# Kernel optimization log

Measured on AMD Instinct MI355X. Metric: run time of the kernel, lower is better.

The kernel has to match this reference:

```python
import jax, jax.numpy as jnp
import numpy as np

B, S, D, H = 2, 2048, 1024, 16
HD = D // H  # 64


def setup_inputs() -> dict:
    key = jax.random.key(0)
    ks = jax.random.split(key, 11)
    sc = 1.0 / np.sqrt(D)
    return {
        "query": jax.random.normal(ks[0], (B, S, D), jnp.float32),
        "key_in": jax.random.normal(ks[1], (B, S, D), jnp.float32),
        "value_in": jax.random.normal(ks[2], (B, S, D), jnp.float32),
        "mask": jnp.ones((1, 1, S, S), dtype=bool),
        "Wq": jax.random.normal(ks[3], (D, D), jnp.float32) * sc,
        "bq": jnp.zeros((D,), jnp.float32),
        "Wk": jax.random.normal(ks[4], (D, D), jnp.float32) * sc,
        "bk": jnp.zeros((D,), jnp.float32),
        "Wv": jax.random.normal(ks[5], (D, D), jnp.float32) * sc,
        "bv": jnp.zeros((D,), jnp.float32),
        "Wo": jax.random.normal(ks[6], (D, D), jnp.float32) * sc,
        "bo": jnp.zeros((D,), jnp.float32),
    }


def _split_heads(x):
    b, s, _ = x.shape
    return x.reshape(b, s, H, HD).transpose(0, 2, 1, 3)  # [B,H,S,HD]


def reference(query, key_in, value_in, mask, Wq, bq, Wk, bk, Wv, bv, Wo, bo):
    # linear projections (torch Linear: x @ W.T + b)
    q = _split_heads(query @ Wq.T + bq)
    k = _split_heads(key_in @ Wk.T + bk)
    v = _split_heads(value_in @ Wv.T + bv)
    scores = jnp.einsum("bhqd,bhkd->bhqk", q, k) / np.sqrt(HD).astype(np.float32)
    scores = jnp.where(mask == 0, jnp.float32(-1e20), scores)
    probs = jax.nn.softmax(scores, axis=-1)
    attn = jnp.einsum("bhqk,bhkd->bhqd", probs, v)  # [B,H,S,HD]
    combined = attn.transpose(0, 2, 1, 3).reshape(query.shape[0], query.shape[1], H * HD)
    return combined @ Wo.T + bo
```

## Files before the change

kernel.cpp:

```cpp
#include <hip/hip_runtime.h>

#define B_  2
#define S_  2048
#define D_  1024
#define H_  16
#define HD_ 64

typedef float          f32x4 __attribute__((ext_vector_type(4)));
typedef short          s16x8 __attribute__((ext_vector_type(8)));
typedef unsigned short u16x4 __attribute__((ext_vector_type(4)));

static __device__ __forceinline__ unsigned short f2bf(float f) {
  unsigned int u = __builtin_bit_cast(unsigned int, f);
  u += 0x7FFFu + ((u >> 16) & 1u);
  return (unsigned short)(u >> 16);
}

#define GLDS16(g, l)                                                        \
  __builtin_amdgcn_global_load_lds(                                         \
      (const __attribute__((address_space(1))) void*)(g),                   \
      (__attribute__((address_space(3))) void*)(l), 16, 0, 0)

#define XF(r) (((((r) >> 4) & 3) * 16) ^ ((((r) & 7)) * 8))
#define XP(r) ((((r) >> 2) & 3) * 16)

struct ConvSet {
  const float* s[7];
  unsigned short* d[7];
  int n[7];
};

__global__ __launch_bounds__(256) void conv_kernel(ConvSet cs) {
  const int idx = blockIdx.y;
  const int i = (blockIdx.x * 256 + threadIdx.x) * 8;
  if (i >= cs.n[idx]) return;
  const float* s = cs.s[idx];
  unsigned short* d = cs.d[idx];
  f32x4 a = *(const f32x4*)(s + i);
  f32x4 b = *(const f32x4*)(s + i + 4);
  u16x4 pa, pb;
#pragma unroll
  for (int j = 0; j < 4; ++j) { pa[j] = f2bf(a[j]); pb[j] = f2bf(b[j]); }
  *(u16x4*)(d + i) = pa;
  *(u16x4*)(d + i + 4) = pb;
}

template <bool PERM>
__global__ __launch_bounds__(256) void gemm_bf16(
    const unsigned short* __restrict__ X0, const unsigned short* __restrict__ X1,
    const unsigned short* __restrict__ X2,
    const unsigned short* __restrict__ W0, const unsigned short* __restrict__ W1,
    const unsigned short* __restrict__ W2,
    const float* __restrict__ b0, const float* __restrict__ b1, const float* __restrict__ b2,
    void* __restrict__ o0, void* __restrict__ o1, void* __restrict__ o2)
{
  constexpr int K = D_, N = D_;
  const int z = blockIdx.z;
  const unsigned short* X = z == 0 ? X0 : (z == 1 ? X1 : X2);
  const unsigned short* W = z == 0 ? W0 : (z == 1 ? W1 : W2);
  const float* bias       = z == 0 ? b0 : (z == 1 ? b1 : b2);
  void* outp              = z == 0 ? o0 : (z == 1 ? o1 : o2);

  __shared__ unsigned short As[128][32];
  __shared__ unsigned short Bs[128][32];

  const int t = threadIdx.x, lane = t & 63, w = t >> 6;
  const int wr = w >> 1, wc = w & 1;
  const int m0 = blockIdx.y * 128, n0 = blockIdx.x * 128;
  const int lg = lane >> 4, lr = lane & 15;

  const int srow = w * 32 + (lane >> 2);
  const int scol = (lane & 3) * 8;
  const unsigned short* Asrc = X + (size_t)(m0 + srow) * K + scol;
  const unsigned short* Bsrc = W + (size_t)(n0 + srow) * K + scol;

  f32x4 acc[4][4];
#pragma unroll
  for (int i = 0; i < 4; ++i)
#pragma unroll
    for (int j = 0; j < 4; ++j) acc[i][j] = f32x4{0.f, 0.f, 0.f, 0.f};

  for (int k0 = 0; k0 < K; k0 += 32) {
    __syncthreads();
#pragma unroll
    for (int i = 0; i < 2; ++i) {
      GLDS16(Asrc + k0 + (size_t)i * 16 * K, &As[w * 32 + i * 16][0]);
      GLDS16(Bsrc + k0 + (size_t)i * 16 * K, &Bs[w * 32 + i * 16][0]);
    }
    __syncthreads();

    s16x8 af[4], bfr[4];
#pragma unroll
    for (int i = 0; i < 4; ++i) af[i]  = *(const s16x8*)&As[wr * 64 + i * 16 + lr][lg * 8];
#pragma unroll
    for (int j = 0; j < 4; ++j) bfr[j] = *(const s16x8*)&Bs[wc * 64 + j * 16 + lr][lg * 8];
#pragma unroll
    for (int i = 0; i < 4; ++i)
#pragma unroll
      for (int j = 0; j < 4; ++j)
        acc[i][j] = __builtin_amdgcn_mfma_f32_16x16x32_bf16(af[i], bfr[j], acc[i][j], 0, 0, 0);
  }

#pragma unroll
  for (int i = 0; i < 4; ++i) {
    int rowb = m0 + wr * 64 + i * 16 + lg * 4;
#pragma unroll
    for (int j = 0; j < 4; ++j) {
      int col = n0 + wc * 64 + j * 16 + lr;
      float bv = bias[col];
#pragma unroll
      for (int r = 0; r < 4; ++r) {
        float v = acc[i][j][r] + bv;
        int rr = rowb + r;
        if (PERM) {
          int b = rr >> 11, s = rr & (S_ - 1);
          int h = col >> 6, hd = col & (HD_ - 1);
          ((unsigned short*)outp)[(((size_t)(b * H_ + h)) * S_ + s) * HD_ + hd] = f2bf(v);
        } else {
          ((float*)outp)[(size_t)rr * N + col] = v;
        }
      }
    }
  }
}

template <bool XF32, bool PERM>
__global__ __launch_bounds__(256) void gemm_kernel(
    const void* __restrict__ X0, const void* __restrict__ X1, const void* __restrict__ X2,
    const float* __restrict__ W0, const float* __restrict__ W1, const float* __restrict__ W2,
    const float* __restrict__ b0, const float* __restrict__ b1, const float* __restrict__ b2,
    void* __restrict__ o0, void* __restrict__ o1, void* __restrict__ o2)
{
  constexpr int K = D_, N = D_;
  const int z = blockIdx.z;
  const void*  Xv   = z == 0 ? X0 : (z == 1 ? X1 : X2);
  const float* W    = z == 0 ? W0 : (z == 1 ? W1 : W2);
  const float* bias = z == 0 ? b0 : (z == 1 ? b1 : b2);
  void*        outp = z == 0 ? o0 : (z == 1 ? o1 : o2);

  __shared__ unsigned short As[128][32];
  __shared__ unsigned short Bs[128][32];

  const int t = threadIdx.x, lane = t & 63, w = t >> 6;
  const int wr = w >> 1, wc = w & 1;
  const int m0 = blockIdx.y * 128, n0 = blockIdx.x * 128;
  const int lg = lane >> 4, lr = lane & 15;

  f32x4 acc[4][4];
#pragma unroll
  for (int i = 0; i < 4; ++i)
#pragma unroll
    for (int j = 0; j < 4; ++j) acc[i][j] = f32x4{0.f, 0.f, 0.f, 0.f};

  for (int k0 = 0; k0 < K; k0 += 32) {
    __syncthreads();
#pragma unroll
    for (int i = 0; i < 4; ++i) {
      int c = t + 256 * i;
      int row = c >> 3, ko = (c & 7) * 4;
      if (XF32) {
        const float* Xf = (const float*)Xv;
        f32x4 v = *(const f32x4*)(Xf + (size_t)(m0 + row) * K + k0 + ko);
        u16x4 p;
#pragma unroll
        for (int j = 0; j < 4; ++j) p[j] = f2bf(v[j]);
        *(u16x4*)&As[row][ko] = p;
      } else {
        const unsigned short* Xu = (const unsigned short*)Xv;
        *(u16x4*)&As[row][ko] = *(const u16x4*)(Xu + (size_t)(m0 + row) * K + k0 + ko);
      }
    }
#pragma unroll
    for (int i = 0; i < 4; ++i) {
      int c = t + 256 * i;
      int row = c >> 3, ko = (c & 7) * 4;
      f32x4 v = *(const f32x4*)(W + (size_t)(n0 + row) * K + k0 + ko);
      u16x4 p;
#pragma unroll
      for (int j = 0; j < 4; ++j) p[j] = f2bf(v[j]);
      *(u16x4*)&Bs[row][ko] = p;
    }
    __syncthreads();

    s16x8 af[4], bfr[4];
#pragma unroll
    for (int i = 0; i < 4; ++i) af[i]  = *(const s16x8*)&As[wr * 64 + i * 16 + lr][lg * 8];
#pragma unroll
    for (int j = 0; j < 4; ++j) bfr[j] = *(const s16x8*)&Bs[wc * 64 + j * 16 + lr][lg * 8];
#pragma unroll
    for (int i = 0; i < 4; ++i)
#pragma unroll
      for (int j = 0; j < 4; ++j)
        acc[i][j] = __builtin_amdgcn_mfma_f32_16x16x32_bf16(af[i], bfr[j], acc[i][j], 0, 0, 0);
  }

#pragma unroll
  for (int i = 0; i < 4; ++i) {
    int rowb = m0 + wr * 64 + i * 16 + lg * 4;
#pragma unroll
    for (int j = 0; j < 4; ++j) {
      int col = n0 + wc * 64 + j * 16 + lr;
      float bv = bias[col];
#pragma unroll
      for (int r = 0; r < 4; ++r) {
        float v = acc[i][j][r] + bv;
        int rr = rowb + r;
        if (PERM) {
          int b = rr >> 11, s = rr & (S_ - 1);
          int h = col >> 6, hd = col & (HD_ - 1);
          ((unsigned short*)outp)[(((size_t)(b * H_ + h)) * S_ + s) * HD_ + hd] = f2bf(v);
        } else {
          ((float*)outp)[(size_t)rr * N + col] = v;
        }
      }
    }
  }
}

__global__ __launch_bounds__(256) void attn_kernel(
    const unsigned short* __restrict__ Q,
    const unsigned short* __restrict__ Kg,
    const unsigned short* __restrict__ V,
    unsigned short* __restrict__ O)
{
  __shared__ unsigned short Ks[64][64];
  __shared__ unsigned short Vt[64][64];
  __shared__ unsigned short Pw[4][16][64];

  const int t = threadIdx.x, lane = t & 63, w = t >> 6;
  const int lg = lane >> 4, lr = lane & 15;
  const int bh = blockIdx.y;
  const int q0 = blockIdx.x * 64 + w * 16;
  const size_t base = (size_t)bh * S_ * HD_;

  s16x8 qa[2];
#pragma unroll
  for (int kc = 0; kc < 2; ++kc)
    qa[kc] = *(const s16x8*)(Q + base + (size_t)(q0 + lr) * HD_ + kc * 32 + lg * 8);

  const int cg = (lane & 7) ^ ((w & 3) * 2) ^ ((lane >> 3) & 7);
  const unsigned short* Ksrc0 =
      Kg + base + (size_t)(w * 16 + (lane >> 3)) * HD_ + cg * 8;

  const int sr = t >> 2;
  const int sc = (t & 3) * 16;
  const unsigned short* Vsrc0 = V + base + (size_t)sr * HD_ + sc;
  int vcol0[8], vcol1[8];
#pragma unroll
  for (int j = 0; j < 8; ++j) {
    vcol0[j] = sr ^ XF(sc + j);
    vcol1[j] = sr ^ XF(sc + 8 + j);
  }

  f32x4 po[4];
#pragma unroll
  for (int nb = 0; nb < 4; ++nb) po[nb] = f32x4{0.f, 0.f, 0.f, 0.f};
  float m_r[4], l_r[4];
#pragma unroll
  for (int r = 0; r < 4; ++r) { m_r[r] = -1e30f; l_r[r] = 0.f; }

  const float C2 = 0.18033688f;

  for (int kt = 0; kt < S_ / 64; ++kt) {
    __syncthreads();
    {
      const size_t toff = (size_t)kt * 64 * HD_;
      GLDS16(Ksrc0 + toff, &Ks[w * 16][0]);
      GLDS16(Ksrc0 + toff + 8 * HD_, &Ks[w * 16 + 8][0]);
      s16x8 v0 = *(const s16x8*)(Vsrc0 + toff);
      s16x8 v1 = *(const s16x8*)(Vsrc0 + toff + 8);
#pragma unroll
      for (int j = 0; j < 8; ++j) {
        Vt[sc + j][vcol0[j]]     = (unsigned short)v0[j];
        Vt[sc + 8 + j][vcol1[j]] = (unsigned short)v1[j];
      }
    }
    __syncthreads();

    f32x4 sf[4];
#pragma unroll
    for (int nb = 0; nb < 4; ++nb) {
      f32x4 a = f32x4{0.f, 0.f, 0.f, 0.f};
      int row = nb * 16 + lr;
      int xr = XF(row);
#pragma unroll
      for (int kc = 0; kc < 2; ++kc) {
        s16x8 kb = *(const s16x8*)&Ks[row][(kc * 32 + lg * 8) ^ xr];
        a = __builtin_amdgcn_mfma_f32_16x16x32_bf16(qa[kc], kb, a, 0, 0, 0);
      }
      sf[nb] = a;
    }

    float pr[4][4], mx[4];
#pragma unroll
    for (int r = 0; r < 4; ++r) {
      float s0 = sf[0][r] * C2, s1 = sf[1][r] * C2;
      float s2 = sf[2][r] * C2, s3 = sf[3][r] * C2;
      pr[0][r] = s0; pr[1][r] = s1; pr[2][r] = s2; pr[3][r] = s3;
      mx[r] = fmaxf(fmaxf(s0, s1), fmaxf(s2, s3));
    }
#pragma unroll
    for (int off = 8; off >= 1; off >>= 1)
#pragma unroll
      for (int r = 0; r < 4; ++r) mx[r] = fmaxf(mx[r], __shfl_xor(mx[r], off));

    bool grow = false;
#pragma unroll
    for (int r = 0; r < 4; ++r) grow = grow || (mx[r] > m_r[r] + 8.f);
    if (__any(grow)) {
#pragma unroll
      for (int r = 0; r < 4; ++r) {
        float mn = fmaxf(m_r[r], mx[r]);
        float alpha = __builtin_amdgcn_exp2f(m_r[r] - mn);
        m_r[r] = mn;
        l_r[r] *= alpha;
#pragma unroll
        for (int nb = 0; nb < 4; ++nb) po[nb][r] *= alpha;
      }
    }

    float rs[4];
#pragma unroll
    for (int r = 0; r < 4; ++r) {
      float a0 = __builtin_amdgcn_exp2f(pr[0][r] - m_r[r]);
      float a1 = __builtin_amdgcn_exp2f(pr[1][r] - m_r[r]);
      float a2 = __builtin_amdgcn_exp2f(pr[2][r] - m_r[r]);
      float a3 = __builtin_amdgcn_exp2f(pr[3][r] - m_r[r]);
      pr[0][r] = a0; pr[1][r] = a1; pr[2][r] = a2; pr[3][r] = a3;
      rs[r] = (a0 + a1) + (a2 + a3);
    }
#pragma unroll
    for (int off = 8; off >= 1; off >>= 1)
#pragma unroll
      for (int r = 0; r < 4; ++r) rs[r] += __shfl_xor(rs[r], off);
#pragma unroll
    for (int r = 0; r < 4; ++r) l_r[r] += rs[r];

#pragma unroll
    for (int nb = 0; nb < 4; ++nb)
#pragma unroll
      for (int r = 0; r < 4; ++r) {
        int row = lg * 4 + r;
        Pw[w][row][(nb * 16 + lr) ^ XP(row)] = f2bf(pr[nb][r]);
      }
    asm volatile("s_waitcnt lgkmcnt(0)" ::: "memory");
    __builtin_amdgcn_sched_barrier(0);
    s16x8 pa[2];
#pragma unroll
    for (int kc = 0; kc < 2; ++kc)
      pa[kc] = *(const s16x8*)&Pw[w][lr][(kc * 32 + lg * 8) ^ XP(lr)];

#pragma unroll
    for (int nb = 0; nb < 4; ++nb) {
      int d = nb * 16 + lr;
      int xd = XF(d);
#pragma unroll
      for (int kc = 0; kc < 2; ++kc) {
        s16x8 vb = *(const s16x8*)&Vt[d][(kc * 32 + lg * 8) ^ xd];
        po[nb] = __builtin_amdgcn_mfma_f32_16x16x32_bf16(pa[kc], vb, po[nb], 0, 0, 0);
      }
    }
  }

  const int b = bh >> 4, h = bh & (H_ - 1);
  float inv[4];
#pragma unroll
  for (int r = 0; r < 4; ++r) inv[r] = __builtin_amdgcn_rcpf(l_r[r]);
#pragma unroll
  for (int nb = 0; nb < 4; ++nb)
#pragma unroll
    for (int r = 0; r < 4; ++r) {
      int q = q0 + lg * 4 + r;
      int d = nb * 16 + lr;
      O[((size_t)(b * S_ + q)) * D_ + h * HD_ + d] = f2bf(po[nb][r] * inv[r]);
    }
}

extern "C" void kernel_launch(void* const* d_in, const int* in_sizes, int n_in,
                              void* d_out, int out_size, void* d_ws, size_t ws_size,
                              hipStream_t stream) {
  const float* query    = (const float*)d_in[0];
  const float* key_in   = (const float*)d_in[1];
  const float* value_in = (const float*)d_in[2];
  const float* Wq = (const float*)d_in[4];
  const float* bq = (const float*)d_in[5];
  const float* Wk = (const float*)d_in[6];
  const float* bk = (const float*)d_in[7];
  const float* Wv = (const float*)d_in[8];
  const float* bv = (const float*)d_in[9];
  const float* Wo = (const float*)d_in[10];
  const float* bo = (const float*)d_in[11];

  const size_t NA = (size_t)B_ * S_ * D_;
  const size_t NW = (size_t)D_ * D_;
  dim3 blk(256);

  if (ws_size >= (7 * NA + 4 * NW) * sizeof(unsigned short)) {
    unsigned short* Xb[3];
    Xb[0] = (unsigned short*)d_ws;
    Xb[1] = Xb[0] + NA;
    Xb[2] = Xb[1] + NA;
    unsigned short* Wb[4];
    Wb[0] = Xb[2] + NA;
    Wb[1] = Wb[0] + NW;
    Wb[2] = Wb[1] + NW;
    Wb[3] = Wb[2] + NW;
    unsigned short* Qp = Wb[3] + NW;
    unsigned short* Kp = Qp + NA;
    unsigned short* Vp = Kp + NA;
    unsigned short* Ao = Vp + NA;

    ConvSet cs;
    cs.s[0] = query;    cs.d[0] = Xb[0]; cs.n[0] = (int)NA;
    cs.s[1] = key_in;   cs.d[1] = Xb[1]; cs.n[1] = (int)NA;
    cs.s[2] = value_in; cs.d[2] = Xb[2]; cs.n[2] = (int)NA;
    cs.s[3] = Wq; cs.d[3] = Wb[0]; cs.n[3] = (int)NW;
    cs.s[4] = Wk; cs.d[4] = Wb[1]; cs.n[4] = (int)NW;
    cs.s[5] = Wv; cs.d[5] = Wb[2]; cs.n[5] = (int)NW;
    cs.s[6] = Wo; cs.d[6] = Wb[3]; cs.n[6] = (int)NW;
    conv_kernel<<<dim3((unsigned)(NA / (256 * 8)), 7), blk, 0, stream>>>(cs);

    gemm_bf16<true><<<dim3(8, 32, 3), blk, 0, stream>>>(
        Xb[0], Xb[1], Xb[2], Wb[0], Wb[1], Wb[2], bq, bk, bv, Qp, Kp, Vp);
    attn_kernel<<<dim3(S_ / 64, B_ * H_), blk, 0, stream>>>(Qp, Kp, Vp, Ao);
    gemm_bf16<false><<<dim3(8, 32, 1), blk, 0, stream>>>(
        Ao, nullptr, nullptr, Wb[3], nullptr, nullptr, bo, nullptr, nullptr,
        (float*)d_out, nullptr, nullptr);
  } else {
    unsigned short* Qp = (unsigned short*)d_ws;
    unsigned short* Kp = Qp + NA;
    unsigned short* Vp = Kp + NA;
    unsigned short* Ao = Vp + NA;
    gemm_kernel<true, true><<<dim3(8, 32, 3), blk, 0, stream>>>(
        query, key_in, value_in, Wq, Wk, Wv, bq, bk, bv, Qp, Kp, Vp);
    attn_kernel<<<dim3(S_ / 64, B_ * H_), blk, 0, stream>>>(Qp, Kp, Vp, Ao);
    gemm_kernel<false, false><<<dim3(8, 32, 1), blk, 0, stream>>>(
        Ao, nullptr, nullptr, Wo, nullptr, nullptr, bo, nullptr, nullptr,
        (float*)d_out, nullptr, nullptr);
  }
}
```

Before: 305.8 us.

## Fuse activation bf16 conversion into QKV GEMM, pre-transpose V, double-buffer attention

The QKV projection GEMM now reads fp32 activations directly and converts them to bf16 while staging into shared memory. This removes the separate conversion pass over the three activation tensors and its workspace traffic. The V projection is written transposed ([d][s]), so the attention kernel can load V tiles asynchronously with global_load_lds instead of scattering a transpose through LDS. Attention now double-buffers its K/V tiles, swaps MFMA operand order so each lane owns one query row (simplifying max/sum reductions), and packs P stores and the output write through LDS for coalesced 16-byte global stores. The fallback gemm_kernel's epilogue was also changed so its V output is transposed, which the fallback attention path now expects. The trade-offs are uncoalesced fp32 activation loads in the GEMM main loop and more LDS use in attention.

```diff
diff --git a/kernel.cpp b/kernel.cpp
--- a/kernel.cpp
+++ b/kernel.cpp
@@ -9,6 +9,7 @@
 typedef float          f32x4 __attribute__((ext_vector_type(4)));
 typedef short          s16x8 __attribute__((ext_vector_type(8)));
 typedef unsigned short u16x4 __attribute__((ext_vector_type(4)));
+typedef unsigned int   u32x4 __attribute__((ext_vector_type(4)));
 
 static __device__ __forceinline__ unsigned short f2bf(float f) {
   unsigned int u = __builtin_bit_cast(unsigned int, f);
@@ -21,13 +22,10 @@
       (const __attribute__((address_space(1))) void*)(g),                   \
       (__attribute__((address_space(3))) void*)(l), 16, 0, 0)
 
-#define XF(r) (((((r) >> 4) & 3) * 16) ^ ((((r) & 7)) * 8))
-#define XP(r) ((((r) >> 2) & 3) * 16)
-
 struct ConvSet {
-  const float* s[7];
-  unsigned short* d[7];
-  int n[7];
+  const float* s[4];
+  unsigned short* d[4];
+  int n[4];
 };
 
 __global__ __launch_bounds__(256) void conv_kernel(ConvSet cs) {
@@ -45,10 +43,10 @@
   *(u16x4*)(d + i + 4) = pb;
 }
 
-template <bool PERM>
+template <int XM, bool PERM>
 __global__ __launch_bounds__(256) void gemm_bf16(
-    const unsigned short* __restrict__ X0, const unsigned short* __restrict__ X1,
-    const unsigned short* __restrict__ X2,
+    const void* __restrict__ X0, const void* __restrict__ X1,
+    const void* __restrict__ X2,
     const unsigned short* __restrict__ W0, const unsigned short* __restrict__ W1,
     const unsigned short* __restrict__ W2,
     const float* __restrict__ b0, const float* __restrict__ b1, const float* __restrict__ b2,
@@ -56,7 +54,7 @@
 {
   constexpr int K = D_, N = D_;
   const int z = blockIdx.z;
-  const unsigned short* X = z == 0 ? X0 : (z == 1 ? X1 : X2);
+  const void* X           = z == 0 ? X0 : (z == 1 ? X1 : X2);
   const unsigned short* W = z == 0 ? W0 : (z == 1 ? W1 : W2);
   const float* bias       = z == 0 ? b0 : (z == 1 ? b1 : b2);
   void* outp              = z == 0 ? o0 : (z == 1 ? o1 : o2);
@@ -71,8 +69,9 @@
 
   const int srow = w * 32 + (lane >> 2);
   const int scol = (lane & 3) * 8;
-  const unsigned short* Asrc = X + (size_t)(m0 + srow) * K + scol;
   const unsigned short* Bsrc = W + (size_t)(n0 + srow) * K + scol;
+  const unsigned short* Asrc =
+      (XM == 0) ? (const unsigned short*)X + (size_t)(m0 + srow) * K + scol : nullptr;
 
   f32x4 acc[4][4];
 #pragma unroll
@@ -82,11 +81,26 @@
 
   for (int k0 = 0; k0 < K; k0 += 32) {
     __syncthreads();
-#pragma unroll
-    for (int i = 0; i < 2; ++i) {
-      GLDS16(Asrc + k0 + (size_t)i * 16 * K, &As[w * 32 + i * 16][0]);
+    if (XM == 0) {
+#pragma unroll
+      for (int i = 0; i < 2; ++i)
+        GLDS16(Asrc + k0 + (size_t)i * 16 * K, &As[w * 32 + i * 16][0]);
+    } else {
+      const float* Xf = (const float*)X;
+#pragma unroll
+      for (int i = 0; i < 4; ++i) {
+        int c = t + 256 * i;
+        int row = c >> 3, ko = (c & 7) * 4;
+        f32x4 v = *(const f32x4*)(Xf + (size_t)(m0 + row) * K + k0 + ko);
+        u16x4 p;
+#pragma unroll
+        for (int j = 0; j < 4; ++j) p[j] = f2bf(v[j]);
+        *(u16x4*)&As[row][ko] = p;
+      }
+    }
+#pragma unroll
+    for (int i = 0; i < 2; ++i)
       GLDS16(Bsrc + k0 + (size_t)i * 16 * K, &Bs[w * 32 + i * 16][0]);
-    }
     __syncthreads();
 
     s16x8 af[4], bfr[4];
@@ -108,17 +122,27 @@
     for (int j = 0; j < 4; ++j) {
       int col = n0 + wc * 64 + j * 16 + lr;
       float bv = bias[col];
-#pragma unroll
-      for (int r = 0; r < 4; ++r) {
-        float v = acc[i][j][r] + bv;
-        int rr = rowb + r;
-        if (PERM) {
-          int b = rr >> 11, s = rr & (S_ - 1);
-          int h = col >> 6, hd = col & (HD_ - 1);
-          ((unsigned short*)outp)[(((size_t)(b * H_ + h)) * S_ + s) * HD_ + hd] = f2bf(v);
+      if (PERM) {
+        unsigned short* o = (unsigned short*)outp;
+        int h = col >> 6, hd = col & (HD_ - 1);
+        if (z == 2) {
+          int b = rowb >> 11, sv = rowb & (S_ - 1);
+          u16x4 pv;
+#pragma unroll
+          for (int r = 0; r < 4; ++r) pv[r] = f2bf(acc[i][j][r] + bv);
+          *(u16x4*)(o + ((size_t)((b * H_ + h) * HD_ + hd)) * S_ + sv) = pv;
         } else {
-          ((float*)outp)[(size_t)rr * N + col] = v;
+#pragma unroll
+          for (int r = 0; r < 4; ++r) {
+            int rr = rowb + r;
+            int b = rr >> 11, s = rr & (S_ - 1);
+            o[(((size_t)(b * H_ + h)) * S_ + s) * HD_ + hd] = f2bf(acc[i][j][r] + bv);
+          }
         }
+      } else {
+#pragma unroll
+        for (int r = 0; r < 4; ++r)
+          ((float*)outp)[(size_t)(rowb + r) * N + col] = acc[i][j][r] + bv;
       }
     }
   }
@@ -201,17 +225,27 @@
     for (int j = 0; j < 4; ++j) {
       int col = n0 + wc * 64 + j * 16 + lr;
       float bv = bias[col];
-#pragma unroll
-      for (int r = 0; r < 4; ++r) {
-        float v = acc[i][j][r] + bv;
-        int rr = rowb + r;
-        if (PERM) {
-          int b = rr >> 11, s = rr & (S_ - 1);
-          int h = col >> 6, hd = col & (HD_ - 1);
-          ((unsigned short*)outp)[(((size_t)(b * H_ + h)) * S_ + s) * HD_ + hd] = f2bf(v);
+      if (PERM) {
+        unsigned short* o = (unsigned short*)outp;
+        int h = col >> 6, hd = col & (HD_ - 1);
+        if (z == 2) {
+          int b = rowb >> 11, sv = rowb & (S_ - 1);
+          u16x4 pv;
+#pragma unroll
+          for (int r = 0; r < 4; ++r) pv[r] = f2bf(acc[i][j][r] + bv);
+          *(u16x4*)(o + ((size_t)((b * H_ + h) * HD_ + hd)) * S_ + sv) = pv;
         } else {
-          ((float*)outp)[(size_t)rr * N + col] = v;
+#pragma unroll
+          for (int r = 0; r < 4; ++r) {
+            int rr = rowb + r;
+            int b = rr >> 11, s = rr & (S_ - 1);
+            o[(((size_t)(b * H_ + h)) * S_ + s) * HD_ + hd] = f2bf(acc[i][j][r] + bv);
+          }
         }
+      } else {
+#pragma unroll
+        for (int r = 0; r < 4; ++r)
+          ((float*)outp)[(size_t)(rowb + r) * N + col] = acc[i][j][r] + bv;
       }
     }
   }
@@ -220,160 +254,160 @@
 __global__ __launch_bounds__(256) void attn_kernel(
     const unsigned short* __restrict__ Q,
     const unsigned short* __restrict__ Kg,
-    const unsigned short* __restrict__ V,
+    const unsigned short* __restrict__ VT,
     unsigned short* __restrict__ O)
 {
-  __shared__ unsigned short Ks[64][64];
-  __shared__ unsigned short Vt[64][64];
-  __shared__ unsigned short Pw[4][16][64];
+  __shared__ unsigned short Ks[2][64][64];
+  __shared__ unsigned short Vt[2][64][64];
+  __shared__ unsigned int   Pw32[4][16][32];
 
   const int t = threadIdx.x, lane = t & 63, w = t >> 6;
   const int lg = lane >> 4, lr = lane & 15;
   const int bh = blockIdx.y;
   const int q0 = blockIdx.x * 64 + w * 16;
-  const size_t base = (size_t)bh * S_ * HD_;
+  const size_t baseK = (size_t)bh * S_ * HD_;
+  const size_t baseV = (size_t)bh * HD_ * S_;
 
   s16x8 qa[2];
 #pragma unroll
   for (int kc = 0; kc < 2; ++kc)
-    qa[kc] = *(const s16x8*)(Q + base + (size_t)(q0 + lr) * HD_ + kc * 32 + lg * 8);
-
-  const int cg = (lane & 7) ^ ((w & 3) * 2) ^ ((lane >> 3) & 7);
-  const unsigned short* Ksrc0 =
-      Kg + base + (size_t)(w * 16 + (lane >> 3)) * HD_ + cg * 8;
-
-  const int sr = t >> 2;
-  const int sc = (t & 3) * 16;
-  const unsigned short* Vsrc0 = V + base + (size_t)sr * HD_ + sc;
-  int vcol0[8], vcol1[8];
-#pragma unroll
-  for (int j = 0; j < 8; ++j) {
-    vcol0[j] = sr ^ XF(sc + j);
-    vcol1[j] = sr ^ XF(sc + 8 + j);
-  }
+    qa[kc] = *(const s16x8*)(Q + baseK + (size_t)(q0 + lr) * HD_ + kc * 32 + lg * 8);
+
+  const int sub = lane >> 3;
+  const int cg  = (lane & 7) ^ sub;
+  const unsigned short* Ksrc = Kg + baseK + (size_t)(w * 16 + sub) * HD_ + cg * 8;
+  const unsigned short* Vsrc = VT + baseV + (size_t)(w * 16 + sub) * S_  + cg * 8;
 
   f32x4 po[4];
 #pragma unroll
   for (int nb = 0; nb < 4; ++nb) po[nb] = f32x4{0.f, 0.f, 0.f, 0.f};
-  float m_r[4], l_r[4];
-#pragma unroll
-  for (int r = 0; r < 4; ++r) { m_r[r] = -1e30f; l_r[r] = 0.f; }
-
+  float m_r = -1e30f, l_r = 0.f;
   const float C2 = 0.18033688f;
-
-  for (int kt = 0; kt < S_ / 64; ++kt) {
-    __syncthreads();
-    {
-      const size_t toff = (size_t)kt * 64 * HD_;
-      GLDS16(Ksrc0 + toff, &Ks[w * 16][0]);
-      GLDS16(Ksrc0 + toff + 8 * HD_, &Ks[w * 16 + 8][0]);
-      s16x8 v0 = *(const s16x8*)(Vsrc0 + toff);
-      s16x8 v1 = *(const s16x8*)(Vsrc0 + toff + 8);
-#pragma unroll
-      for (int j = 0; j < 8; ++j) {
-        Vt[sc + j][vcol0[j]]     = (unsigned short)v0[j];
-        Vt[sc + 8 + j][vcol1[j]] = (unsigned short)v1[j];
-      }
-    }
-    __syncthreads();
+  const int   xs = (lr & 7) * 8;
+  const int   xw = (lr & 7) * 4;
+
+  constexpr int NT = S_ / 64;
+
+  {
+    GLDS16(Ksrc,                    &Ks[0][w * 16][0]);
+    GLDS16(Ksrc + 8 * HD_,          &Ks[0][w * 16 + 8][0]);
+    GLDS16(Vsrc,                    &Vt[0][w * 16][0]);
+    GLDS16(Vsrc + (size_t)8 * S_,   &Vt[0][w * 16 + 8][0]);
+  }
+  __syncthreads();
+
+  for (int kt = 0; kt < NT; ++kt) {
+    const int cur = kt & 1;
+    if (kt + 1 < NT) {
+      const int nxt = cur ^ 1;
+      const size_t ko = (size_t)(kt + 1) * 64 * HD_;
+      const size_t vo = (size_t)(kt + 1) * 64;
+      GLDS16(Ksrc + ko,                  &Ks[nxt][w * 16][0]);
+      GLDS16(Ksrc + ko + 8 * HD_,        &Ks[nxt][w * 16 + 8][0]);
+      GLDS16(Vsrc + vo,                  &Vt[nxt][w * 16][0]);
+      GLDS16(Vsrc + vo + (size_t)8 * S_, &Vt[nxt][w * 16 + 8][0]);
+    }
 
     f32x4 sf[4];
 #pragma unroll
     for (int nb = 0; nb < 4; ++nb) {
       f32x4 a = f32x4{0.f, 0.f, 0.f, 0.f};
       int row = nb * 16 + lr;
-      int xr = XF(row);
 #pragma unroll
       for (int kc = 0; kc < 2; ++kc) {
-        s16x8 kb = *(const s16x8*)&Ks[row][(kc * 32 + lg * 8) ^ xr];
-        a = __builtin_amdgcn_mfma_f32_16x16x32_bf16(qa[kc], kb, a, 0, 0, 0);
+        s16x8 kb = *(const s16x8*)&Ks[cur][row][(kc * 32 + lg * 8) ^ xs];
+        a = __builtin_amdgcn_mfma_f32_16x16x32_bf16(kb, qa[kc], a, 0, 0, 0);
       }
       sf[nb] = a;
     }
 
-    float pr[4][4], mx[4];
-#pragma unroll
-    for (int r = 0; r < 4; ++r) {
-      float s0 = sf[0][r] * C2, s1 = sf[1][r] * C2;
-      float s2 = sf[2][r] * C2, s3 = sf[3][r] * C2;
-      pr[0][r] = s0; pr[1][r] = s1; pr[2][r] = s2; pr[3][r] = s3;
-      mx[r] = fmaxf(fmaxf(s0, s1), fmaxf(s2, s3));
-    }
-#pragma unroll
-    for (int off = 8; off >= 1; off >>= 1)
-#pragma unroll
-      for (int r = 0; r < 4; ++r) mx[r] = fmaxf(mx[r], __shfl_xor(mx[r], off));
-
-    bool grow = false;
-#pragma unroll
-    for (int r = 0; r < 4; ++r) grow = grow || (mx[r] > m_r[r] + 8.f);
+    float mx = sf[0][0];
+#pragma unroll
+    for (int nb = 0; nb < 4; ++nb)
+#pragma unroll
+      for (int r = 0; r < 4; ++r) mx = fmaxf(mx, sf[nb][r]);
+    mx = fmaxf(mx, __shfl_xor(mx, 16));
+    mx = fmaxf(mx, __shfl_xor(mx, 32));
+    float ms = mx * C2;
+    bool grow = (ms - m_r) > 8.f;
     if (__any(grow)) {
+      float mn = fmaxf(m_r, ms);
+      float alpha = __builtin_amdgcn_exp2f(m_r - mn);
+      m_r = mn;
+      l_r *= alpha;
+#pragma unroll
+      for (int nb = 0; nb < 4; ++nb)
+#pragma unroll
+        for (int r = 0; r < 4; ++r) po[nb][r] *= alpha;
+    }
+
+    float pr[4][4];
+    float rs = 0.f;
+#pragma unroll
+    for (int nb = 0; nb < 4; ++nb)
 #pragma unroll
       for (int r = 0; r < 4; ++r) {
-        float mn = fmaxf(m_r[r], mx[r]);
-        float alpha = __builtin_amdgcn_exp2f(m_r[r] - mn);
-        m_r[r] = mn;
-        l_r[r] *= alpha;
-#pragma unroll
-        for (int nb = 0; nb < 4; ++nb) po[nb][r] *= alpha;
-      }
-    }
-
-    float rs[4];
-#pragma unroll
-    for (int r = 0; r < 4; ++r) {
-      float a0 = __builtin_amdgcn_exp2f(pr[0][r] - m_r[r]);
-      float a1 = __builtin_amdgcn_exp2f(pr[1][r] - m_r[r]);
-      float a2 = __builtin_amdgcn_exp2f(pr[2][r] - m_r[r]);
-      float a3 = __builtin_amdgcn_exp2f(pr[3][r] - m_r[r]);
-      pr[0][r] = a0; pr[1][r] = a1; pr[2][r] = a2; pr[3][r] = a3;
-      rs[r] = (a0 + a1) + (a2 + a3);
-    }
-#pragma unroll
-    for (int off = 8; off >= 1; off >>= 1)
-#pragma unroll
-      for (int r = 0; r < 4; ++r) rs[r] += __shfl_xor(rs[r], off);
-#pragma unroll
-    for (int r = 0; r < 4; ++r) l_r[r] += rs[r];
+        float p = __builtin_amdgcn_exp2f(fmaf(sf[nb][r], C2, -m_r));
+        pr[nb][r] = p;
+        rs += p;
+      }
+    rs += __shfl_xor(rs, 16);
+    rs += __shfl_xor(rs, 32);
+    l_r += rs;
 
 #pragma unroll
     for (int nb = 0; nb < 4; ++nb)
 #pragma unroll
-      for (int r = 0; r < 4; ++r) {
-        int row = lg * 4 + r;
-        Pw[w][row][(nb * 16 + lr) ^ XP(row)] = f2bf(pr[nb][r]);
+      for (int half = 0; half < 2; ++half) {
+        unsigned pk = (unsigned)f2bf(pr[nb][2 * half]) |
+                      ((unsigned)f2bf(pr[nb][2 * half + 1]) << 16);
+        Pw32[w][lr][(nb * 8 + lg * 2 + half) ^ xw] = pk;
       }
     asm volatile("s_waitcnt lgkmcnt(0)" ::: "memory");
     __builtin_amdgcn_sched_barrier(0);
     s16x8 pa[2];
 #pragma unroll
     for (int kc = 0; kc < 2; ++kc)
-      pa[kc] = *(const s16x8*)&Pw[w][lr][(kc * 32 + lg * 8) ^ XP(lr)];
+      pa[kc] = *(const s16x8*)&Pw32[w][lr][(kc * 16 + lg * 4) ^ xw];
 
 #pragma unroll
     for (int nb = 0; nb < 4; ++nb) {
       int d = nb * 16 + lr;
-      int xd = XF(d);
 #pragma unroll
       for (int kc = 0; kc < 2; ++kc) {
-        s16x8 vb = *(const s16x8*)&Vt[d][(kc * 32 + lg * 8) ^ xd];
-        po[nb] = __builtin_amdgcn_mfma_f32_16x16x32_bf16(pa[kc], vb, po[nb], 0, 0, 0);
-      }
-    }
-  }
-
-  const int b = bh >> 4, h = bh & (H_ - 1);
-  float inv[4];
-#pragma unroll
-  for (int r = 0; r < 4; ++r) inv[r] = __builtin_amdgcn_rcpf(l_r[r]);
-#pragma unroll
-  for (int nb = 0; nb < 4; ++nb)
-#pragma unroll
-    for (int r = 0; r < 4; ++r) {
-      int q = q0 + lg * 4 + r;
-      int d = nb * 16 + lr;
-      O[((size_t)(b * S_ + q)) * D_ + h * HD_ + d] = f2bf(po[nb][r] * inv[r]);
-    }
+        s16x8 vb = *(const s16x8*)&Vt[cur][d][(kc * 32 + lg * 8) ^ xs];
+        po[nb] = __builtin_amdgcn_mfma_f32_16x16x32_bf16(vb, pa[kc], po[nb], 0, 0, 0);
+      }
+    }
+
+    __syncthreads();
+  }
+
+  unsigned* Ot = (unsigned*)&Ks[0][0][0];
+  {
+    float inv = __builtin_amdgcn_rcpf(l_r);
+    const int qlocal = w * 16 + lr;
+#pragma unroll
+    for (int nb = 0; nb < 4; ++nb)
+#pragma unroll
+      for (int half = 0; half < 2; ++half) {
+        unsigned pk = (unsigned)f2bf(po[nb][2 * half] * inv) |
+                      ((unsigned)f2bf(po[nb][2 * half + 1] * inv) << 16);
+        Ot[qlocal * 32 + ((nb * 8 + lg * 2 + half) ^ xw)] = pk;
+      }
+  }
+  __syncthreads();
+  {
+    const int qp = t >> 2, ch = t & 3;
+    const int xq = (qp & 7) * 4;
+    u32x4 r0 = *(const u32x4*)&Ot[qp * 32 + ((ch * 8) ^ xq)];
+    u32x4 r1 = *(const u32x4*)&Ot[qp * 32 + ((ch * 8 + 4) ^ xq)];
+    const int b = bh >> 4, h = bh & (H_ - 1);
+    size_t s = (size_t)blockIdx.x * 64 + qp;
+    unsigned short* o = O + ((size_t)b * S_ + s) * D_ + h * HD_ + ch * 16;
+    *(u32x4*)o = r0;
+    *(u32x4*)(o + 8) = r1;
+  }
 }
 
 extern "C" void kernel_launch(void* const* d_in, const int* in_sizes, int n_in,
@@ -395,13 +429,9 @@
   const size_t NW = (size_t)D_ * D_;
   dim3 blk(256);
 
-  if (ws_size >= (7 * NA + 4 * NW) * sizeof(unsigned short)) {
-    unsigned short* Xb[3];
-    Xb[0] = (unsigned short*)d_ws;
-    Xb[1] = Xb[0] + NA;
-    Xb[2] = Xb[1] + NA;
+  if (ws_size >= (4 * NA + 4 * NW) * sizeof(unsigned short)) {
     unsigned short* Wb[4];
-    Wb[0] = Xb[2] + NA;
+    Wb[0] = (unsigned short*)d_ws;
     Wb[1] = Wb[0] + NW;
     Wb[2] = Wb[1] + NW;
     Wb[3] = Wb[2] + NW;
@@ -411,19 +441,16 @@
     unsigned short* Ao = Vp + NA;
 
     ConvSet cs;
-    cs.s[0] = query;    cs.d[0] = Xb[0]; cs.n[0] = (int)NA;
-    cs.s[1] = key_in;   cs.d[1] = Xb[1]; cs.n[1] = (int)NA;
-    cs.s[2] = value_in; cs.d[2] = Xb[2]; cs.n[2] = (int)NA;
-    cs.s[3] = Wq; cs.d[3] = Wb[0]; cs.n[3] = (int)NW;
-    cs.s[4] = Wk; cs.d[4] = Wb[1]; cs.n[4] = (int)NW;
-    cs.s[5] = Wv; cs.d[5] = Wb[2]; cs.n[5] = (int)NW;
-    cs.s[6] = Wo; cs.d[6] = Wb[3]; cs.n[6] = (int)NW;
-    conv_kernel<<<dim3((unsigned)(NA / (256 * 8)), 7), blk, 0, stream>>>(cs);
-
-    gemm_bf16<true><<<dim3(8, 32, 3), blk, 0, stream>>>(
-        Xb[0], Xb[1], Xb[2], Wb[0], Wb[1], Wb[2], bq, bk, bv, Qp, Kp, Vp);
+    cs.s[0] = Wq; cs.d[0] = Wb[0]; cs.n[0] = (int)NW;
+    cs.s[1] = Wk; cs.d[1] = Wb[1]; cs.n[1] = (int)NW;
+    cs.s[2] = Wv; cs.d[2] = Wb[2]; cs.n[2] = (int)NW;
+    cs.s[3] = Wo; cs.d[3] = Wb[3]; cs.n[3] = (int)NW;
+    conv_kernel<<<dim3((unsigned)(NW / (256 * 8)), 4), blk, 0, stream>>>(cs);
+
+    gemm_bf16<1, true><<<dim3(8, 32, 3), blk, 0, stream>>>(
+        query, key_in, value_in, Wb[0], Wb[1], Wb[2], bq, bk, bv, Qp, Kp, Vp);
     attn_kernel<<<dim3(S_ / 64, B_ * H_), blk, 0, stream>>>(Qp, Kp, Vp, Ao);
-    gemm_bf16<false><<<dim3(8, 32, 1), blk, 0, stream>>>(
+    gemm_bf16<0, false><<<dim3(8, 32, 1), blk, 0, stream>>>(
         Ao, nullptr, nullptr, Wb[3], nullptr, nullptr, bo, nullptr, nullptr,
         (float*)d_out, nullptr, nullptr);
   } else {
```

New measurement: 302.6 us. No clear change (-1.0%).
